# Kernel tuning notes

Measured on AMD Instinct MI355X. Metric: run time of the kernel, lower is better.

## Reference

```python
import jax, jax.numpy as jnp
import numpy as np

N_HEADS = 32
N_KV_HEADS = 8
HEAD_DIM = 128


def setup_inputs() -> dict:
    key = jax.random.key(0)
    ks = jax.random.split(key, 7)
    B, S, D = 2, 2048, 4096
    scale = 0.02
    x = jax.random.normal(ks[0], (B, S, D), dtype=jnp.float32)
    wq = jax.random.normal(ks[1], (D, D), dtype=jnp.float32) * scale
    wk = jax.random.normal(ks[2], (N_KV_HEADS * HEAD_DIM, D), dtype=jnp.float32) * scale
    wv = jax.random.normal(ks[3], (N_KV_HEADS * HEAD_DIM, D), dtype=jnp.float32) * scale
    wo = jax.random.normal(ks[4], (D, D), dtype=jnp.float32) * scale
    # RoPE frequencies: theta = 10000^{-2i/d}, angles = pos * theta
    inv_freq = 1.0 / (10000.0 ** (jnp.arange(0, HEAD_DIM, 2, dtype=jnp.float32) / HEAD_DIM))
    angles = jnp.arange(S, dtype=jnp.float32)[:, None] * inv_freq[None, :]  # (S, HEAD_DIM//2)
    freqs_cos = jnp.cos(angles)
    freqs_sin = jnp.sin(angles)
    # causal additive mask (0 on/below diagonal, -inf above)
    neg_inf = jnp.finfo(jnp.float32).min
    mask = jnp.where(jnp.triu(jnp.ones((S, S), dtype=bool), k=1), neg_inf, 0.0)[None, None]
    return {"x": x, "wq": wq, "wk": wk, "wv": wv, "wo": wo,
            "freqs_cos": freqs_cos, "freqs_sin": freqs_sin, "mask": mask,
            "start_pos": 0}


def _apply_rope(t, cos, sin):
    # t: (B, S, H, D); cos/sin: (S, D//2) -> broadcast (1, S, 1, D//2)
    b, s, h, d = t.shape
    tr = t.reshape(b, s, h, d // 2, 2)
    te, to = tr[..., 0], tr[..., 1]
    c = cos[None, :, None, :]
    si = sin[None, :, None, :]
    out = jnp.stack([te * c - to * si, te * si + to * c], axis=-1)
    return out.reshape(b, s, h, d)


def reference(x, wq, wk, wv, wo, freqs_cos, freqs_sin, mask, start_pos):
    b, s, d = x.shape
    n_rep = N_HEADS // N_KV_HEADS
    xq = (x @ wq.T).reshape(b, s, N_HEADS, HEAD_DIM)
    xk = (x @ wk.T).reshape(b, s, N_KV_HEADS, HEAD_DIM)
    xv = (x @ wv.T).reshape(b, s, N_KV_HEADS, HEAD_DIM)
    xq = _apply_rope(xq, freqs_cos, freqs_sin)
    xk = _apply_rope(xk, freqs_cos, freqs_sin)
    # repeat_kv: (B, S, Hkv, D) -> (B, S, Hkv*n_rep, D)
    keys = jnp.broadcast_to(xk[:, :, :, None, :], (b, s, N_KV_HEADS, n_rep, HEAD_DIM)).reshape(b, s, N_HEADS, HEAD_DIM)
    values = jnp.broadcast_to(xv[:, :, :, None, :], (b, s, N_KV_HEADS, n_rep, HEAD_DIM)).reshape(b, s, N_HEADS, HEAD_DIM)
    q = xq.transpose(0, 2, 1, 3)       # (B, H, S, D)
    k = keys.transpose(0, 2, 1, 3)
    v = values.transpose(0, 2, 1, 3)
    scores = jnp.einsum("bhqd,bhkd->bhqk", q, k) / np.sqrt(HEAD_DIM).astype(np.float32)
    scores = scores + mask
    probs = jax.nn.softmax(scores.astype(jnp.float32), axis=-1).astype(q.dtype)
    out = jnp.einsum("bhqk,bhkd->bhqd", probs, v)
    out = out.transpose(0, 2, 1, 3).reshape(b, s, N_HEADS * HEAD_DIM)
    return out @ wo.T
```

## Files before the change

kernel.cpp:

```cpp
#include <hip/hip_runtime.h>
#include <cstdint>
#include <cstddef>

#define B_  2
#define S_  2048
#define D_  4096
#define NH  32
#define NKV 8
#define HD  128

typedef unsigned short u16;
typedef unsigned int   u32;
typedef __attribute__((ext_vector_type(8))) short short8;
typedef __attribute__((ext_vector_type(4))) float f32x4;

__device__ __forceinline__ u16 f2bf(float f) {
  u32 u = __float_as_uint(f);
  u32 r = (u + 0x7FFFu + ((u >> 16) & 1u)) >> 16;
  return (u16)r;
}
__device__ __forceinline__ float bf2f(u32 lo16) {
  return __uint_as_float(lo16 << 16);
}
__device__ __forceinline__ u32 cvtpk_bf16(float lo, float hi) {
  u32 r;
  asm("v_cvt_pk_bf16_f32 %0, %1, %2" : "=v"(r) : "v"(lo), "v"(hi));
  return r;
}
__device__ __forceinline__ void load_lds16(const void* g, void* lds) {
  __builtin_amdgcn_global_load_lds(
      (const __attribute__((address_space(1))) u32*)g,
      (__attribute__((address_space(3))) u32*)lds, 16, 0, 0);
}

__global__ __launch_bounds__(256) void f32_to_bf16_k(const float* __restrict__ src,
                                                     u16* __restrict__ dst, int n8) {
  int i = blockIdx.x * 256 + threadIdx.x;
  if (i >= n8) return;
  const float4* s = (const float4*)src + (size_t)i * 2;
  float4 a = s[0], b = s[1];
  u32 w0 = (u32)f2bf(a.x) | ((u32)f2bf(a.y) << 16);
  u32 w1 = (u32)f2bf(a.z) | ((u32)f2bf(a.w) << 16);
  u32 w2 = (u32)f2bf(b.x) | ((u32)f2bf(b.y) << 16);
  u32 w3 = (u32)f2bf(b.z) | ((u32)f2bf(b.w) << 16);
  uint4 o; o.x = w0; o.y = w1; o.z = w2; o.w = w3;
  *((uint4*)dst + i) = o;
}

template <int MODE, bool ROPE>
__global__ __launch_bounds__(512, 2)
void gemm256(const u16* __restrict__ A, const u16* __restrict__ Bw,
             void* __restrict__ Cout, int M, int N, int K, int Hh,
             const float* __restrict__ fc, const float* __restrict__ fs) {
  const int tid = threadIdx.x, lid = tid & 63, w = tid >> 6;
  const int lr = lid & 15, lg = lid >> 4;
  const int wm = w >> 2, wn = w & 3;

  int lin = blockIdx.y * gridDim.x + blockIdx.x;
  int bm, bn;
  if (gridDim.x == 16 && gridDim.y == 16) {
    int xcd = lin & 7, idx = lin >> 3;
    bm = ((xcd & 3) * 4 + (idx >> 3)) * 256;
    bn = ((xcd >> 2) * 8 + (idx & 7)) * 256;
  } else {
    bm = blockIdx.y * 256;
    bn = blockIdx.x * 256;
  }

  __shared__ __align__(16) u16 Al[2][2][8192];
  __shared__ __align__(16) u16 Bl[2][2][8192];

  f32x4 acc[8][4];
#pragma unroll
  for (int i = 0; i < 8; ++i)
#pragma unroll
    for (int j = 0; j < 4; ++j) acc[i][j] = (f32x4){0.f, 0.f, 0.f, 0.f};


#define STG_A(B2, KS, K0)                                                       \
  do {                                                                          \
    _Pragma("unroll")                                                           \
    for (int j_ = 0; j_ < 2; ++j_) {                                            \
      int c_ = j_ * 512 + tid;                                                  \
      int r_ = c_ >> 2, cb_ = c_ & 3;                                           \
      int s_ = (cb_ ^ (r_ >> 1)) & 3;                                           \
      load_lds16(A + (size_t)(bm + r_) * K + (K0) + (KS) * 32 + s_ * 8,         \
                 &Al[B2][KS][c_ * 8]);                                          \
    }                                                                           \
  } while (0)
#define STG_B(B2, KS, K0)                                                       \
  do {                                                                          \
    _Pragma("unroll")                                                           \
    for (int j_ = 0; j_ < 2; ++j_) {                                            \
      int c_ = j_ * 512 + tid;                                                  \
      int r_ = c_ >> 2, cb_ = c_ & 3;                                           \
      int s_ = (cb_ ^ (r_ >> 1)) & 3;                                           \
      load_lds16(Bw + (size_t)(bn + r_) * K + (K0) + (KS) * 32 + s_ * 8,        \
                 &Bl[B2][KS][c_ * 8]);                                          \
    }                                                                           \
  } while (0)

  const int nt = K >> 6;
  STG_A(0, 0, 0); STG_B(0, 0, 0); STG_A(0, 1, 0); STG_B(0, 1, 0);
  asm volatile("s_waitcnt vmcnt(4)" ::: "memory");
  __builtin_amdgcn_s_barrier();

  for (int t = 0; t < nt; ++t) {
    const int buf = t & 1, b2 = buf ^ 1;
    const int k1 = (t + 1) << 6;
    const bool pf = (t + 1 < nt);
    short8 a[4], bfr[4];

#pragma unroll
    for (int ni = 0; ni < 4; ++ni) {
      int r = wn * 64 + ni * 16 + lr;
      bfr[ni] = *(const short8*)&Bl[buf][0][r * 32 + ((lg ^ (r >> 1)) & 3) * 8];
    }
#pragma unroll
    for (int mi = 0; mi < 4; ++mi) {
      int r = wm * 128 + mi * 16 + lr;
      a[mi] = *(const short8*)&Al[buf][0][r * 32 + ((lg ^ (r >> 1)) & 3) * 8];
    }
    if (pf) STG_A(b2, 0, k1);
    __builtin_amdgcn_s_barrier();
    __builtin_amdgcn_s_setprio(1);
#pragma unroll
    for (int mi = 0; mi < 4; ++mi)
#pragma unroll
      for (int ni = 0; ni < 4; ++ni)
        acc[mi][ni] = __builtin_amdgcn_mfma_f32_16x16x32_bf16(a[mi], bfr[ni], acc[mi][ni], 0, 0, 0);
    __builtin_amdgcn_s_setprio(0);

#pragma unroll
    for (int mi = 0; mi < 4; ++mi) {
      int r = wm * 128 + (mi + 4) * 16 + lr;
      a[mi] = *(const short8*)&Al[buf][0][r * 32 + ((lg ^ (r >> 1)) & 3) * 8];
    }
    if (pf) STG_B(b2, 0, k1);
    __builtin_amdgcn_s_barrier();
    __builtin_amdgcn_s_setprio(1);
#pragma unroll
    for (int mi = 0; mi < 4; ++mi)
#pragma unroll
      for (int ni = 0; ni < 4; ++ni)
        acc[mi + 4][ni] = __builtin_amdgcn_mfma_f32_16x16x32_bf16(a[mi], bfr[ni], acc[mi + 4][ni], 0, 0, 0);
    __builtin_amdgcn_s_setprio(0);

    if (pf) asm volatile("s_waitcnt vmcnt(4)" ::: "memory");
    else    asm volatile("s_waitcnt vmcnt(0)" ::: "memory");
    __builtin_amdgcn_s_barrier();

#pragma unroll
    for (int ni = 0; ni < 4; ++ni) {
      int r = wn * 64 + ni * 16 + lr;
      bfr[ni] = *(const short8*)&Bl[buf][1][r * 32 + ((lg ^ (r >> 1)) & 3) * 8];
    }
#pragma unroll
    for (int mi = 0; mi < 4; ++mi) {
      int r = wm * 128 + mi * 16 + lr;
      a[mi] = *(const short8*)&Al[buf][1][r * 32 + ((lg ^ (r >> 1)) & 3) * 8];
    }
    if (pf) STG_A(b2, 1, k1);
    __builtin_amdgcn_s_barrier();
    __builtin_amdgcn_s_setprio(1);
#pragma unroll
    for (int mi = 0; mi < 4; ++mi)
#pragma unroll
      for (int ni = 0; ni < 4; ++ni)
        acc[mi][ni] = __builtin_amdgcn_mfma_f32_16x16x32_bf16(a[mi], bfr[ni], acc[mi][ni], 0, 0, 0);
    __builtin_amdgcn_s_setprio(0);

#pragma unroll
    for (int mi = 0; mi < 4; ++mi) {
      int r = wm * 128 + (mi + 4) * 16 + lr;
      a[mi] = *(const short8*)&Al[buf][1][r * 32 + ((lg ^ (r >> 1)) & 3) * 8];
    }
    if (pf) STG_B(b2, 1, k1);
    __builtin_amdgcn_s_barrier();
    __builtin_amdgcn_s_setprio(1);
#pragma unroll
    for (int mi = 0; mi < 4; ++mi)
#pragma unroll
      for (int ni = 0; ni < 4; ++ni)
        acc[mi + 4][ni] = __builtin_amdgcn_mfma_f32_16x16x32_bf16(a[mi], bfr[ni], acc[mi + 4][ni], 0, 0, 0);
    __builtin_amdgcn_s_setprio(0);

    if (pf) {
      asm volatile("s_waitcnt vmcnt(4)" ::: "memory");
      __builtin_amdgcn_s_barrier();
    }
  }
#undef STG_A
#undef STG_B

#pragma unroll
  for (int mi = 0; mi < 8; ++mi)
#pragma unroll
    for (int ni = 0; ni < 4; ++ni)
#pragma unroll
      for (int v = 0; v < 4; ++v) {
        int m = bm + wm * 128 + mi * 16 + lg * 4 + v;
        int n = bn + wn * 64 + ni * 16 + lr;
        float val = acc[mi][ni][v];
        if (ROPE) {
          int srow = m & (S_ - 1);
          int j = (n & (HD - 1)) >> 1;
          float c = fc[(size_t)srow * 64 + j];
          float s = fs[(size_t)srow * 64 + j];
          float partner = __shfl_xor(val, 1);
          val = (n & 1) ? (val * c + partner * s) : (val * c - partner * s);
        }
        if (MODE == 0) {
          ((float*)Cout)[(size_t)m * N + n] = val;
        } else if (MODE == 1) {
          int b = m >> 11, s = m & (S_ - 1), hh = n >> 7, d = n & (HD - 1);
          ((u16*)Cout)[(((size_t)(b * Hh + hh)) * S_ + s) * HD + d] = f2bf(val);
        } else {
          int b = m >> 11, s = m & (S_ - 1), hh = n >> 7, d = n & (HD - 1);
          ((u16*)Cout)[(((size_t)(b * Hh + hh)) * HD + d) * S_ + s] = f2bf(val);
        }
      }
}

template <int MODE, bool ROPE>
__global__ __launch_bounds__(256)
void gemm_bt(const u16* __restrict__ A, const u16* __restrict__ Bw,
             void* __restrict__ Cout, int M, int N, int K, int Hh,
             const float* __restrict__ fc, const float* __restrict__ fs) {
  const int tid = threadIdx.x;
  const int lid = tid & 63, w = tid >> 6;
  const int lr = lid & 15, lg = lid >> 4;
  const int wm = w >> 1, wn = w & 1;

  const int gx = gridDim.x;
  const int nwg = gx * gridDim.y;
  const int lin = blockIdx.y * gx + blockIdx.x;
  const int cpx = nwg >> 3;
  const int lin2 = (lin & 7) * cpx + (lin >> 3);
  const int bm = (lin2 / gx) * 128, bn = (lin2 % gx) * 128;

  __shared__ __align__(16) u16 Al[128 * 64];
  __shared__ __align__(16) u16 Bl[128 * 64];
  f32x4 acc[4][4];
#pragma unroll
  for (int i = 0; i < 4; ++i)
#pragma unroll
    for (int j = 0; j < 4; ++j) acc[i][j] = (f32x4){0.f, 0.f, 0.f, 0.f};

  for (int k0 = 0; k0 < K; k0 += 64) {
    __syncthreads();
#pragma unroll
    for (int i = 0; i < 4; ++i) {
      int c = i * 256 + tid;
      int row = c >> 3, cb = c & 7;
      int cbs = (cb ^ row) & 7;
      load_lds16(A + (size_t)(bm + row) * K + k0 + cbs * 8, &Al[c * 8]);
    }
#pragma unroll
    for (int i = 0; i < 4; ++i) {
      int c = i * 256 + tid;
      int row = c >> 3, cb = c & 7;
      int cbs = (cb ^ row) & 7;
      load_lds16(Bw + (size_t)(bn + row) * K + k0 + cbs * 8, &Bl[c * 8]);
    }
    __syncthreads();
#pragma unroll
    for (int ks = 0; ks < 2; ++ks) {
      short8 af[4], bf[4];
#pragma unroll
      for (int mi = 0; mi < 4; ++mi) {
        int row = wm * 64 + mi * 16 + lr;
        af[mi] = *(const short8*)&Al[row * 64 + (((ks * 4 + lg) ^ row) & 7) * 8];
      }
#pragma unroll
      for (int ni = 0; ni < 4; ++ni) {
        int row = wn * 64 + ni * 16 + lr;
        bf[ni] = *(const short8*)&Bl[row * 64 + (((ks * 4 + lg) ^ row) & 7) * 8];
      }
#pragma unroll
      for (int mi = 0; mi < 4; ++mi)
#pragma unroll
        for (int ni = 0; ni < 4; ++ni)
          acc[mi][ni] = __builtin_amdgcn_mfma_f32_16x16x32_bf16(af[mi], bf[ni], acc[mi][ni], 0, 0, 0);
    }
  }
#pragma unroll
  for (int mi = 0; mi < 4; ++mi)
#pragma unroll
    for (int ni = 0; ni < 4; ++ni)
#pragma unroll
      for (int v = 0; v < 4; ++v) {
        int m = bm + wm * 64 + mi * 16 + lg * 4 + v;
        int n = bn + wn * 64 + ni * 16 + lr;
        float val = acc[mi][ni][v];
        if (ROPE) {
          int srow = m & (S_ - 1);
          int j = (n & (HD - 1)) >> 1;
          float c = fc[(size_t)srow * 64 + j];
          float s = fs[(size_t)srow * 64 + j];
          float partner = __shfl_xor(val, 1);
          val = (n & 1) ? (val * c + partner * s) : (val * c - partner * s);
        }
        if (MODE == 0) {
          ((float*)Cout)[(size_t)m * N + n] = val;
        } else if (MODE == 1) {
          int b = m >> 11, s = m & (S_ - 1), hh = n >> 7, d = n & (HD - 1);
          ((u16*)Cout)[(((size_t)(b * Hh + hh)) * S_ + s) * HD + d] = f2bf(val);
        } else {
          int b = m >> 11, s = m & (S_ - 1), hh = n >> 7, d = n & (HD - 1);
          ((u16*)Cout)[(((size_t)(b * Hh + hh)) * HD + d) * S_ + s] = f2bf(val);
        }
      }
}

__global__ __launch_bounds__(512, 4)
void attn_k(const u16* __restrict__ Qr, const u16* __restrict__ Kr,
            const u16* __restrict__ Vt, u16* __restrict__ Ao) {
  const int xp = blockIdx.x, h = blockIdx.y, b = blockIdx.z;
  const int kvh = h >> 2;
  const int tid = threadIdx.x, lid = tid & 63, w = tid >> 6;
  const int lr = lid & 15, lg = lid >> 4;
  __shared__ __align__(16) u16 Kl[2][64 * 128];
  __shared__ __align__(16) u16 Vl[2][128 * 64];
  __shared__ __align__(16) u32 Plw[8 * 512];

  const size_t qbase = ((size_t)(b * NH + h)) * S_ * HD;
  const size_t kbase = ((size_t)(b * NKV + kvh)) * S_ * HD;
  const size_t vbase = ((size_t)(b * NKV + kvh)) * HD * S_;
  const float scl = 0.08838834764831845f * 1.44269504088896340f;
  const int pb = w * 512 + lr * 32;
  const int qx = 4 * (lr & 7);

#define STAGE(BUF, KT)                                                              \
  do {                                                                              \
    _Pragma("unroll")                                                               \
    for (int i_ = 0; i_ < 2; ++i_) {                                                \
      int c_ = i_ * 512 + tid;                                                      \
      int row_ = c_ >> 4, cb_ = c_ & 15;                                            \
      int cbs_ = (cb_ & 8) | ((cb_ ^ row_) & 7);                                    \
      load_lds16(&Kr[kbase + (size_t)((KT) + row_) * HD + cbs_ * 8],                \
                 &Kl[BUF][(i_ * 512 + w * 64) * 8]);                                \
    }                                                                               \
    _Pragma("unroll")                                                               \
    for (int i_ = 0; i_ < 2; ++i_) {                                                \
      int c_ = i_ * 512 + tid;                                                      \
      int d_ = c_ >> 3, cb_ = c_ & 7;                                               \
      int cbs_ = (cb_ ^ d_) & 7;                                                    \
      load_lds16(&Vt[vbase + (size_t)d_ * S_ + (KT) + cbs_ * 8],                    \
                 &Vl[BUF][(i_ * 512 + w * 64) * 8]);                                \
    }                                                                               \
  } while (0)

  for (int part = 0; part < 2; ++part) {
    const int qi = part ? xp : (15 - xp);
    const int qb = qi * 128;
    const int ntiles = qi * 2 + 2;
    const int q_abs = qb + w * 16 + lr;

    short8 qf[4];
#pragma unroll
    for (int ks = 0; ks < 4; ++ks)
      qf[ks] = *(const short8*)&Qr[qbase + (size_t)q_abs * HD + ks * 32 + lg * 8];

    float m2 = -3.0e38f, osum = 0.f;
    f32x4 oacc[8];
#pragma unroll
    for (int nd = 0; nd < 8; ++nd) oacc[nd] = (f32x4){0.f, 0.f, 0.f, 0.f};

    STAGE(0, 0);
    __syncthreads();
    int cur = 0;

    for (int t = 0; t < ntiles; ++t) {
      const int kt = t * 64;
      if (t + 1 < ntiles) STAGE(cur ^ 1, kt + 64);

      f32x4 sc[4];
#pragma unroll
      for (int ni = 0; ni < 4; ++ni) sc[ni] = (f32x4){0.f, 0.f, 0.f, 0.f};
      __builtin_amdgcn_s_setprio(1);
#pragma unroll
      for (int ks = 0; ks < 4; ++ks) {
#pragma unroll
        for (int ni = 0; ni < 4; ++ni) {
          int row = ni * 16 + lr;
          int ch = ks * 4 + lg;
          int chs = (ch & 8) | ((ch ^ row) & 7);
          short8 kf = *(const short8*)&Kl[cur][row * 128 + chs * 8];
          sc[ni] = __builtin_amdgcn_mfma_f32_16x16x32_bf16(kf, qf[ks], sc[ni], 0, 0, 0);
        }
      }
      __builtin_amdgcn_s_setprio(0);

      const bool edge = (kt + 64 > qb);
      float mx = -3.0e38f;
#pragma unroll
      for (int ni = 0; ni < 4; ++ni)
#pragma unroll
        for (int v = 0; v < 4; ++v) {
          float s = sc[ni][v] * scl;
          int kv = kt + ni * 16 + lg * 4 + v;
          if (edge && kv > q_abs) s = -3.0e38f;
          sc[ni][v] = s;
          mx = fmaxf(mx, s);
        }
      mx = fmaxf(mx, __shfl_xor(mx, 16));
      mx = fmaxf(mx, __shfl_xor(mx, 32));

      if (__any(mx > m2 + 8.0f)) {
        float mnew = fmaxf(m2, mx);
        float fr = exp2f(m2 - mnew);
        m2 = mnew;
        osum *= fr;
#pragma unroll
        for (int nd = 0; nd < 8; ++nd) oacc[nd] *= fr;
      }

      float ps = 0.f;
#pragma unroll
      for (int ni = 0; ni < 4; ++ni) {
#pragma unroll
        for (int p = 0; p < 2; ++p) {
          float e0 = exp2f(sc[ni][2 * p] - m2);
          float e1 = exp2f(sc[ni][2 * p + 1] - m2);
          ps += e0 + e1;
          Plw[pb + ((8 * ni + 2 * lg + p) ^ qx)] = cvtpk_bf16(e0, e1);
        }
      }
      osum += ps;

      asm volatile("s_waitcnt lgkmcnt(0)" ::: "memory");
      __builtin_amdgcn_sched_barrier(0);

      __builtin_amdgcn_s_setprio(1);
#pragma unroll
      for (int ks = 0; ks < 2; ++ks) {
        short8 pfk = *(const short8*)&Plw[pb + ((16 * ks + 4 * lg) ^ qx)];
#pragma unroll
        for (int nd = 0; nd < 8; ++nd) {
          int rowv = nd * 16 + lr;
          int ch = ks * 4 + lg;
          short8 vf = *(const short8*)&Vl[cur][rowv * 64 + ((ch ^ rowv) & 7) * 8];
          oacc[nd] = __builtin_amdgcn_mfma_f32_16x16x32_bf16(vf, pfk, oacc[nd], 0, 0, 0);
        }
      }
      __builtin_amdgcn_s_setprio(0);
      __syncthreads();
      cur ^= 1;
    }

    float os = osum;
    os += __shfl_xor(os, 16);
    os += __shfl_xor(os, 32);
    const float inv = 1.0f / os;
    const size_t orow = ((size_t)(b * S_ + q_abs)) * D_ + h * HD;
    u32* AoW = (u32*)Ao;
#pragma unroll
    for (int nd = 0; nd < 8; ++nd) {
#pragma unroll
      for (int p = 0; p < 2; ++p) {
        u32 pk = cvtpk_bf16(oacc[nd][2 * p] * inv, oacc[nd][2 * p + 1] * inv);
        AoW[(orow + nd * 16 + lg * 4 + 2 * p) >> 1] = pk;
      }
    }
  }
#undef STAGE
}

extern "C" void kernel_launch(void* const* d_in, const int* in_sizes, int n_in,
                              void* d_out, int out_size, void* d_ws, size_t ws_size,
                              hipStream_t stream) {
  const float* x  = (const float*)d_in[0];
  const float* wq = (const float*)d_in[1];
  const float* wk = (const float*)d_in[2];
  const float* wv = (const float*)d_in[3];
  const float* wo = (const float*)d_in[4];
  const float* fc = (const float*)d_in[5];
  const float* fs = (const float*)d_in[6];

  const size_t SZ_X  = (size_t)B_ * S_ * D_ * 2;
  const size_t SZ_WQ = (size_t)D_ * D_ * 2;
  const size_t SZ_WK = (size_t)NKV * HD * D_ * 2;
  char* ws = (char*)d_ws;
  u16* Xb  = (u16*)(ws);
  u16* Wqb = (u16*)(ws + SZ_X);
  u16* Wkb = (u16*)(ws + SZ_X + SZ_WQ);
  u16* Wvb = (u16*)(ws + SZ_X + SZ_WQ + SZ_WK);
  u16* Wob = (u16*)(ws + SZ_X + SZ_WQ + 2 * SZ_WK);
  u16* Qr  = (u16*)(ws + SZ_X + 2 * SZ_WQ + 2 * SZ_WK);
  u16* Kr  = (u16*)(ws + 2 * SZ_X + 2 * SZ_WQ + 2 * SZ_WK);
  u16* Vt  = (u16*)(ws + 2 * SZ_X + 2 * SZ_WQ + 3 * SZ_WK);
  u16* Ao  = (u16*)(ws + 2 * SZ_X + 2 * SZ_WQ + 4 * SZ_WK);
  const size_t NEEDED = 3 * SZ_X + 2 * SZ_WQ + 4 * SZ_WK;
  if (ws_size < NEEDED) return;

  const int nX = B_ * S_ * D_;
  const int nWQ = D_ * D_;
  const int nWK = NKV * HD * D_;
  f32_to_bf16_k<<<nX / 8 / 256, 256, 0, stream>>>(x, Xb, nX / 8);
  f32_to_bf16_k<<<nWQ / 8 / 256, 256, 0, stream>>>(wq, Wqb, nWQ / 8);
  f32_to_bf16_k<<<nWK / 8 / 256, 256, 0, stream>>>(wk, Wkb, nWK / 8);
  f32_to_bf16_k<<<nWK / 8 / 256, 256, 0, stream>>>(wv, Wvb, nWK / 8);
  f32_to_bf16_k<<<nWQ / 8 / 256, 256, 0, stream>>>(wo, Wob, nWQ / 8);

  gemm256<1, true><<<dim3(16, 16), 512, 0, stream>>>(
      Xb, Wqb, Qr, B_ * S_, D_, D_, NH, fc, fs);
  gemm_bt<1, true><<<dim3((NKV * HD) / 128, (B_ * S_) / 128), 256, 0, stream>>>(
      Xb, Wkb, Kr, B_ * S_, NKV * HD, D_, NKV, fc, fs);
  gemm_bt<2, false><<<dim3((NKV * HD) / 128, (B_ * S_) / 128), 256, 0, stream>>>(
      Xb, Wvb, Vt, B_ * S_, NKV * HD, D_, NKV, nullptr, nullptr);

  attn_k<<<dim3(8, NH, B_), 512, 0, stream>>>(Qr, Kr, Vt, Ao);

  gemm256<0, false><<<dim3(16, 16), 512, 0, stream>>>(
      Ao, Wob, d_out, B_ * S_, D_, D_, 0, nullptr, nullptr);
}
```

Baseline: 599.0 us.

## Merge conversion launches, fuse K/V GEMMs, deepen GEMM256 prefetch pipeline

The five f32-to-bf16 conversion launches become a single kernel that picks its source by global index. The separate K and V projection GEMMs become one launch that uses blockIdx.z to choose the weight and epilogue. The main 256-tile GEMM now prefetches half a K-step further ahead, with adjusted vmcnt waits, to hide more global latency. The changes trade launch count and pipeline depth against a more complex wait pattern and some risk of buffer-reuse hazards.

```diff
diff --git a/kernel.cpp b/kernel.cpp
--- a/kernel.cpp
+++ b/kernel.cpp
@@ -33,18 +33,26 @@
       (__attribute__((address_space(3))) u32*)lds, 16, 0, 0);
 }
 
-__global__ __launch_bounds__(256) void f32_to_bf16_k(const float* __restrict__ src,
-                                                     u16* __restrict__ dst, int n8) {
-  int i = blockIdx.x * 256 + threadIdx.x;
-  if (i >= n8) return;
-  const float4* s = (const float4*)src + (size_t)i * 2;
+__global__ __launch_bounds__(256) void cvt_all(
+    const float* __restrict__ x, const float* __restrict__ wq,
+    const float* __restrict__ wk, const float* __restrict__ wv,
+    const float* __restrict__ wo, u16* __restrict__ Xb, u16* __restrict__ Wqb,
+    u16* __restrict__ Wkb, u16* __restrict__ Wvb, u16* __restrict__ Wob) {
+  long i = (long)blockIdx.x * 256 + threadIdx.x;
+  const float* src; u16* dst; long off;
+  if (i < 2097152L)      { src = x;  dst = Xb;  off = i; }
+  else if (i < 4194304L) { src = wq; dst = Wqb; off = i - 2097152L; }
+  else if (i < 4718592L) { src = wk; dst = Wkb; off = i - 4194304L; }
+  else if (i < 5242880L) { src = wv; dst = Wvb; off = i - 4718592L; }
+  else                   { src = wo; dst = Wob; off = i - 5242880L; }
+  const float4* s = (const float4*)src + off * 2;
   float4 a = s[0], b = s[1];
-  u32 w0 = (u32)f2bf(a.x) | ((u32)f2bf(a.y) << 16);
-  u32 w1 = (u32)f2bf(a.z) | ((u32)f2bf(a.w) << 16);
-  u32 w2 = (u32)f2bf(b.x) | ((u32)f2bf(b.y) << 16);
-  u32 w3 = (u32)f2bf(b.z) | ((u32)f2bf(b.w) << 16);
-  uint4 o; o.x = w0; o.y = w1; o.z = w2; o.w = w3;
-  *((uint4*)dst + i) = o;
+  uint4 o;
+  o.x = (u32)f2bf(a.x) | ((u32)f2bf(a.y) << 16);
+  o.y = (u32)f2bf(a.z) | ((u32)f2bf(a.w) << 16);
+  o.z = (u32)f2bf(b.x) | ((u32)f2bf(b.y) << 16);
+  o.w = (u32)f2bf(b.z) | ((u32)f2bf(b.w) << 16);
+  *((uint4*)dst + off) = o;
 }
 
 template <int MODE, bool ROPE>
@@ -75,7 +83,6 @@
   for (int i = 0; i < 8; ++i)
 #pragma unroll
     for (int j = 0; j < 4; ++j) acc[i][j] = (f32x4){0.f, 0.f, 0.f, 0.f};
-
 
 #define STG_A(B2, KS, K0)                                                       \
   do {                                                                          \
@@ -102,13 +109,14 @@
 
   const int nt = K >> 6;
   STG_A(0, 0, 0); STG_B(0, 0, 0); STG_A(0, 1, 0); STG_B(0, 1, 0);
-  asm volatile("s_waitcnt vmcnt(4)" ::: "memory");
+  STG_A(1, 0, 64); STG_B(1, 0, 64);
+  asm volatile("s_waitcnt vmcnt(8)" ::: "memory");
   __builtin_amdgcn_s_barrier();
 
   for (int t = 0; t < nt; ++t) {
-    const int buf = t & 1, b2 = buf ^ 1;
-    const int k1 = (t + 1) << 6;
-    const bool pf = (t + 1 < nt);
+    const int buf = t & 1, bufN = buf ^ 1;
+    const int k1 = (t + 1) << 6, k2 = (t + 2) << 6;
+    const bool pf1 = (t + 1 < nt), pf2 = (t + 2 < nt);
     short8 a[4], bfr[4];
 
 #pragma unroll
@@ -121,7 +129,7 @@
       int r = wm * 128 + mi * 16 + lr;
       a[mi] = *(const short8*)&Al[buf][0][r * 32 + ((lg ^ (r >> 1)) & 3) * 8];
     }
-    if (pf) STG_A(b2, 0, k1);
+    if (pf1) STG_A(bufN, 1, k1);
     __builtin_amdgcn_s_barrier();
     __builtin_amdgcn_s_setprio(1);
 #pragma unroll
@@ -136,7 +144,7 @@
       int r = wm * 128 + (mi + 4) * 16 + lr;
       a[mi] = *(const short8*)&Al[buf][0][r * 32 + ((lg ^ (r >> 1)) & 3) * 8];
     }
-    if (pf) STG_B(b2, 0, k1);
+    if (pf1) STG_B(bufN, 1, k1);
     __builtin_amdgcn_s_barrier();
     __builtin_amdgcn_s_setprio(1);
 #pragma unroll
@@ -146,8 +154,8 @@
         acc[mi + 4][ni] = __builtin_amdgcn_mfma_f32_16x16x32_bf16(a[mi], bfr[ni], acc[mi + 4][ni], 0, 0, 0);
     __builtin_amdgcn_s_setprio(0);
 
-    if (pf) asm volatile("s_waitcnt vmcnt(4)" ::: "memory");
-    else    asm volatile("s_waitcnt vmcnt(0)" ::: "memory");
+    if (pf1) asm volatile("s_waitcnt vmcnt(8)" ::: "memory");
+    else     asm volatile("s_waitcnt vmcnt(0)" ::: "memory");
     __builtin_amdgcn_s_barrier();
 
 #pragma unroll
@@ -160,7 +168,7 @@
       int r = wm * 128 + mi * 16 + lr;
       a[mi] = *(const short8*)&Al[buf][1][r * 32 + ((lg ^ (r >> 1)) & 3) * 8];
     }
-    if (pf) STG_A(b2, 1, k1);
+    if (pf2) STG_A(buf, 0, k2);
     __builtin_amdgcn_s_barrier();
     __builtin_amdgcn_s_setprio(1);
 #pragma unroll
@@ -175,7 +183,7 @@
       int r = wm * 128 + (mi + 4) * 16 + lr;
       a[mi] = *(const short8*)&Al[buf][1][r * 32 + ((lg ^ (r >> 1)) & 3) * 8];
     }
-    if (pf) STG_B(b2, 1, k1);
+    if (pf2) STG_B(buf, 0, k2);
     __builtin_amdgcn_s_barrier();
     __builtin_amdgcn_s_setprio(1);
 #pragma unroll
@@ -185,8 +193,9 @@
         acc[mi + 4][ni] = __builtin_amdgcn_mfma_f32_16x16x32_bf16(a[mi], bfr[ni], acc[mi + 4][ni], 0, 0, 0);
     __builtin_amdgcn_s_setprio(0);
 
-    if (pf) {
-      asm volatile("s_waitcnt vmcnt(4)" ::: "memory");
+    if (pf1) {
+      if (pf2) asm volatile("s_waitcnt vmcnt(8)" ::: "memory");
+      else     asm volatile("s_waitcnt vmcnt(4)" ::: "memory");
       __builtin_amdgcn_s_barrier();
     }
   }
@@ -222,15 +231,17 @@
       }
 }
 
-template <int MODE, bool ROPE>
 __global__ __launch_bounds__(256)
-void gemm_bt(const u16* __restrict__ A, const u16* __restrict__ Bw,
-             void* __restrict__ Cout, int M, int N, int K, int Hh,
+void gemm_kv(const u16* __restrict__ Xb, const u16* __restrict__ Wk,
+             const u16* __restrict__ Wv, u16* __restrict__ Kr, u16* __restrict__ Vt,
              const float* __restrict__ fc, const float* __restrict__ fs) {
   const int tid = threadIdx.x;
   const int lid = tid & 63, w = tid >> 6;
   const int lr = lid & 15, lg = lid >> 4;
   const int wm = w >> 1, wn = w & 1;
+  const int zz = blockIdx.z;
+  const u16* Bw = zz ? Wv : Wk;
+  const int K = D_, N = NKV * HD;
 
   const int gx = gridDim.x;
   const int nwg = gx * gridDim.y;
@@ -254,7 +265,7 @@
       int c = i * 256 + tid;
       int row = c >> 3, cb = c & 7;
       int cbs = (cb ^ row) & 7;
-      load_lds16(A + (size_t)(bm + row) * K + k0 + cbs * 8, &Al[c * 8]);
+      load_lds16(Xb + (size_t)(bm + row) * K + k0 + cbs * 8, &Al[c * 8]);
     }
 #pragma unroll
     for (int i = 0; i < 4; ++i) {
@@ -293,22 +304,16 @@
         int m = bm + wm * 64 + mi * 16 + lg * 4 + v;
         int n = bn + wn * 64 + ni * 16 + lr;
         float val = acc[mi][ni][v];
-        if (ROPE) {
-          int srow = m & (S_ - 1);
-          int j = (n & (HD - 1)) >> 1;
-          float c = fc[(size_t)srow * 64 + j];
-          float s = fs[(size_t)srow * 64 + j];
+        int b = m >> 11, s = m & (S_ - 1), hh = n >> 7, d = n & (HD - 1);
+        if (zz == 0) {
+          int j = d >> 1;
+          float c = fc[(size_t)s * 64 + j];
+          float sn = fs[(size_t)s * 64 + j];
           float partner = __shfl_xor(val, 1);
-          val = (n & 1) ? (val * c + partner * s) : (val * c - partner * s);
-        }
-        if (MODE == 0) {
-          ((float*)Cout)[(size_t)m * N + n] = val;
-        } else if (MODE == 1) {
-          int b = m >> 11, s = m & (S_ - 1), hh = n >> 7, d = n & (HD - 1);
-          ((u16*)Cout)[(((size_t)(b * Hh + hh)) * S_ + s) * HD + d] = f2bf(val);
+          val = (n & 1) ? (val * c + partner * sn) : (val * c - partner * sn);
+          Kr[(((size_t)(b * NKV + hh)) * S_ + s) * HD + d] = f2bf(val);
         } else {
-          int b = m >> 11, s = m & (S_ - 1), hh = n >> 7, d = n & (HD - 1);
-          ((u16*)Cout)[(((size_t)(b * Hh + hh)) * HD + d) * S_ + s] = f2bf(val);
+          Vt[(((size_t)(b * NKV + hh)) * HD + d) * S_ + s] = f2bf(val);
         }
       }
 }
@@ -494,21 +499,11 @@
   const size_t NEEDED = 3 * SZ_X + 2 * SZ_WQ + 4 * SZ_WK;
   if (ws_size < NEEDED) return;
 
-  const int nX = B_ * S_ * D_;
-  const int nWQ = D_ * D_;
-  const int nWK = NKV * HD * D_;
-  f32_to_bf16_k<<<nX / 8 / 256, 256, 0, stream>>>(x, Xb, nX / 8);
-  f32_to_bf16_k<<<nWQ / 8 / 256, 256, 0, stream>>>(wq, Wqb, nWQ / 8);
-  f32_to_bf16_k<<<nWK / 8 / 256, 256, 0, stream>>>(wk, Wkb, nWK / 8);
-  f32_to_bf16_k<<<nWK / 8 / 256, 256, 0, stream>>>(wv, Wvb, nWK / 8);
-  f32_to_bf16_k<<<nWQ / 8 / 256, 256, 0, stream>>>(wo, Wob, nWQ / 8);
+  cvt_all<<<28672, 256, 0, stream>>>(x, wq, wk, wv, wo, Xb, Wqb, Wkb, Wvb, Wob);
 
   gemm256<1, true><<<dim3(16, 16), 512, 0, stream>>>(
       Xb, Wqb, Qr, B_ * S_, D_, D_, NH, fc, fs);
-  gemm_bt<1, true><<<dim3((NKV * HD) / 128, (B_ * S_) / 128), 256, 0, stream>>>(
-      Xb, Wkb, Kr, B_ * S_, NKV * HD, D_, NKV, fc, fs);
-  gemm_bt<2, false><<<dim3((NKV * HD) / 128, (B_ * S_) / 128), 256, 0, stream>>>(
-      Xb, Wvb, Vt, B_ * S_, NKV * HD, D_, NKV, nullptr, nullptr);
+  gemm_kv<<<dim3(8, 32, 2), 256, 0, stream>>>(Xb, Wkb, Wvb, Kr, Vt, fc, fs);
 
   attn_k<<<dim3(8, NH, B_), 512, 0, stream>>>(Qr, Kr, Vt, Ao);
 
```

New measurement: 522.8 us. 1.15x faster.
